# Kernel optimization log

Measured on AMD Instinct MI355X. Metric: run time of the kernel, lower is better.

## Reference

```python
import jax, jax.numpy as jnp
import numpy as np

NI = 2048   # num_items
H = 1024    # hidden_size per direction
B = 256     # batch
T = 256     # max seq len


def setup_inputs() -> dict:
    key = jax.random.key(0)
    ks = jax.random.split(key, 12)
    # ragged lengths, contiguous end-padding with 0 (pack_padded_sequence semantics)
    lens = jax.random.randint(ks[0], (B,), 1, T + 1)
    items = jax.random.randint(ks[1], (B, T), 1, NI)      # 0 is padding, valid in [1, NI)
    actions = jax.random.randint(ks[2], (B, T), 1, 3)     # 1=wrong, 2=right
    valid = jnp.arange(T)[None, :] < lens[:, None]
    items = jnp.where(valid, items, 0)
    actions = jnp.where(valid, actions, 0)
    targets = jax.random.randint(ks[3], (B,), 0, 2)
    s = 0.05
    # W_ih stored transposed [2*NI, 4H]: rows [0:NI) for item one-hot, [NI:2NI) for action one-hot
    Wt_f = jax.random.normal(ks[4], (2 * NI, 4 * H), jnp.float32) * s
    Whh_f = jax.random.normal(ks[5], (H, 4 * H), jnp.float32) * s   # stored as h @ Whh
    b_f = jax.random.normal(ks[6], (4 * H,), jnp.float32) * s       # b_ih + b_hh combined
    Wt_b = jax.random.normal(ks[7], (2 * NI, 4 * H), jnp.float32) * s
    Whh_b = jax.random.normal(ks[8], (H, 4 * H), jnp.float32) * s
    b_b = jax.random.normal(ks[9], (4 * H,), jnp.float32) * s
    Wfc = jax.random.normal(ks[10], (2 * H, 2), jnp.float32) * s
    bfc = jax.random.normal(ks[11], (2,), jnp.float32) * s
    return {"items": items, "actions": actions, "targets": targets,
            "Wt_f": Wt_f, "Whh_f": Whh_f, "b_f": b_f,
            "Wt_b": Wt_b, "Whh_b": Whh_b, "b_b": b_b,
            "Wfc": Wfc, "bfc": bfc}


def _lstm_dir(items, actions, lens, Wt, Whh, b, reverse):
    # one_hot(items) @ W_ih.T == gather rows of W_ih.T  (no dense one-hot materialized)
    Bn, Tn = items.shape
    Hn = Whh.shape[0]
    valid = jnp.arange(Tn)[:, None] < lens[None, :]   # [T, B]
    it, ac = items.T, actions.T                        # [T, B]
    if reverse:
        it, ac, valid = it[::-1], ac[::-1], valid[::-1]

    def step(carry, xs):
        h, c = carry
        i_t, a_t, v = xs
        x = Wt[i_t] + Wt[NI + a_t] + b                 # [B, 4H]
        g = x + h @ Whh
        i, f, gg, o = jnp.split(g, 4, axis=-1)         # PyTorch gate order i,f,g,o
        i, f, o = jax.nn.sigmoid(i), jax.nn.sigmoid(f), jax.nn.sigmoid(o)
        c_new = f * c + i * jnp.tanh(gg)
        h_new = o * jnp.tanh(c_new)
        vm = v[:, None]
        # packed semantics: padded steps are not processed -> state frozen
        return (jnp.where(vm, h_new, h), jnp.where(vm, c_new, c)), None

    h0 = jnp.zeros((Bn, Hn), Wt.dtype)
    (h, _), _ = jax.lax.scan(step, (h0, h0), (it, ac, valid))
    return h  # final hidden: last valid step (fwd) / step 0 (bwd)


def reference(items, actions, targets, Wt_f, Whh_f, b_f, Wt_b, Whh_b, b_b, Wfc, bfc):
    lens = (items != 0).sum(1)
    hf = _lstm_dir(items, actions, lens, Wt_f, Whh_f, b_f, False)
    hb = _lstm_dir(items, actions, lens, Wt_b, Whh_b, b_b, True)
    h = jnp.stack([hf, hb])                            # [2, B, H] like torch h
    # F.dropout(p=0.5, training=True), deterministic key for reproducibility
    keep = jax.random.bernoulli(jax.random.key(42), 0.5, h.shape)
    h = jnp.where(keep, h * 2.0, 0.0)
    feat = jnp.concatenate([h[0], h[1]], axis=-1)      # [B, 2H]
    logits = feat @ Wfc + bfc                          # [B, 2]
    logp = jax.nn.log_softmax(logits, axis=-1)
    loss = -jnp.take_along_axis(logp, targets[:, None], axis=1).mean()
    return loss
```

## Files before the change

kernel.cpp:

```cpp
#include <hip/hip_runtime.h>
#include <stdint.h>

typedef uint32_t u32;
typedef __bf16 bf16;
typedef bf16 bf16x8 __attribute__((ext_vector_type(8)));
typedef float f32x4 __attribute__((ext_vector_type(4)));

#define B_ 256
#define T_ 256
#define H_ 1024
#define G_ 4096
#define NI_ 2048

static constexpr size_t OFF_W2T = 0;
static constexpr size_t SZ_W2T  = (size_t)2 * G_ * H_ * 2;
static constexpr size_t OFF_H   = OFF_W2T + SZ_W2T;
static constexpr size_t SZ_H    = (size_t)2 * 2 * B_ * H_ * 2;
static constexpr size_t OFF_LENS= OFF_H + SZ_H;
static constexpr size_t OFF_RL  = OFF_LENS + 1024;
static constexpr size_t OFF_BAR = OFF_RL + 1024;
static constexpr size_t SZ_BAR  = 36864 * 4;

static constexpr int LDS_BYTES = 131072;

__device__ __forceinline__ float bf2f(uint16_t b){ return __uint_as_float(((u32)b) << 16); }
__device__ __forceinline__ uint16_t f2bf(float f){
  u32 u = __float_as_uint(f);
  return (uint16_t)((u + 0x7fffu + ((u >> 16) & 1u)) >> 16);
}
__device__ __forceinline__ float sigm(float x){ return 1.f / (1.f + __expf(-x)); }
__device__ __forceinline__ float tanh_(float x){ return 1.f - 2.f / (__expf(2.f * x) + 1.f); }

__device__ __forceinline__ void threefry(u32 k0, u32 k1, u32 x0, u32 x1, u32& o0, u32& o1){
  u32 ks2 = k0 ^ k1 ^ 0x1BD11BDAu;
  x0 += k0; x1 += k1;
#define TFR(r) { x0 += x1; x1 = (x1 << r) | (x1 >> (32 - r)); x1 ^= x0; }
  TFR(13) TFR(15) TFR(26) TFR(6)  x0 += k1;  x1 += ks2 + 1u;
  TFR(17) TFR(29) TFR(16) TFR(24) x0 += ks2; x1 += k0 + 2u;
  TFR(13) TFR(15) TFR(26) TFR(6)  x0 += k0;  x1 += k1 + 3u;
  TFR(17) TFR(29) TFR(16) TFR(24) x0 += k1;  x1 += ks2 + 4u;
  TFR(13) TFR(15) TFR(26) TFR(6)  x0 += ks2; x1 += k0 + 5u;
#undef TFR
  o0 = x0; o1 = x1;
}

__device__ __forceinline__ bool keep_mask(u32 idx){
  u32 o0, o1; threefry(0u, 42u, 0u, idx, o0, o1);
  return ((o0 ^ o1) & 0x80000000u) == 0u;
}

__global__ __launch_bounds__(256) void k_prep_w(const float* __restrict__ whh_f,
                                                const float* __restrict__ whh_b,
                                                uint16_t* __restrict__ w2t){
  int bid = blockIdx.x;
  int d  = bid >> 12;
  int r  = bid & 4095;
  int kt = r >> 7;
  int ct = r & 127;
  const float* W = d ? whh_b : whh_f;
  __shared__ float tile[32][33];
  int tid = threadIdx.x;
  int lr = tid >> 5, lc = tid & 31;
#pragma unroll
  for (int i = 0; i < 4; i++)
    tile[lr + i*8][lc] = W[(size_t)(kt*32 + lr + i*8) * G_ + ct*32 + lc];
  __syncthreads();
  int colLocal = tid >> 3, kseg = tid & 7;
  int col = ct*32 + colLocal;
  int strip = col >> 10;
  int hcol  = col & 1023;
  int vcg = (hcol >> 4)*64 + strip*16 + (hcol & 15);
  size_t base = ((size_t)d * G_ + vcg) * H_ + kt*32 + kseg*4;
  u32 w0 = (u32)f2bf(tile[kseg*4+0][colLocal]) | ((u32)f2bf(tile[kseg*4+1][colLocal]) << 16);
  u32 w1 = (u32)f2bf(tile[kseg*4+2][colLocal]) | ((u32)f2bf(tile[kseg*4+3][colLocal]) << 16);
  uint2 v; v.x = w0; v.y = w1;
  *(uint2*)(w2t + base) = v;
}

__global__ __launch_bounds__(256) void k_init(uint16_t* __restrict__ hbuf,
                                              int* __restrict__ lens,
                                              u32* __restrict__ bar,
                                              const int* __restrict__ items){
  int bid = blockIdx.x, tid = threadIdx.x;
  if (bid == 256){
    int cnt = 0;
    for (int t = 0; t < T_; t++) cnt += (items[(size_t)tid * T_ + t] != 0) ? 1 : 0;
    lens[tid] = cnt;
    return;
  }
  size_t g = (size_t)bid * 256 + tid;
  ((uint4*)hbuf)[g] = make_uint4(0,0,0,0);
  if (tid < 36)
    ((uint4*)bar)[bid*36 + tid] = make_uint4(0,0,0,0);
}

#define A_LOAD(dst, base, IMM) \
  asm volatile("global_load_dwordx4 %0, %1, off offset:%2 sc0 sc1" \
    : "=v"(dst) : "v"(base), "i"(IMM) : "memory")
#define A_WAIT(N, r0, r1) \
  asm volatile("s_waitcnt vmcnt(%2)" : "+v"(r0), "+v"(r1) : "i"(N) : "memory")
#define AISS(j) { A_LOAD(pre0[(j)&15], p0, (j)*64); A_LOAD(pre1[(j)&15], p1, (j)*64); }

#define KS1(kk,st,bb) { \
  acc0[st] = __builtin_amdgcn_mfma_f32_16x16x32_bf16(a0_, bb, acc0[st], 0,0,0); \
  acc1[st] = __builtin_amdgcn_mfma_f32_16x16x32_bf16(a1_, bb, acc1[st], 0,0,0); }

#define KSTEP(kk) { \
  bf16x8 bb0 = *(const bf16x8*)(smem + qoff00 + (((kk)&1)?qd1:qd0) + (((kk)&30)<<6)); \
  bf16x8 bb1 = *(const bf16x8*)(smem + qoff00 + 32768  + (((kk)&1)?qd1:qd0) + (((kk)&30)<<6)); \
  bf16x8 bb2 = *(const bf16x8*)(smem + qoff00 + 65536  + (((kk)&1)?qd1:qd0) + (((kk)&30)<<6)); \
  bf16x8 bb3 = *(const bf16x8*)(smem + qoff00 + 98304  + (((kk)&1)?qd1:qd0) + (((kk)&30)<<6)); \
  A_WAIT(((kk)<=16 ? 30 : 62-2*(kk)), pre0[(kk)&15], pre1[(kk)&15]); \
  bf16x8 a0_ = pre0[(kk)&15]; bf16x8 a1_ = pre1[(kk)&15]; \
  KS1(kk,0,bb0) KS1(kk,1,bb1) KS1(kk,2,bb2) KS1(kk,3,bb3) \
  if ((kk) < 16) { AISS((kk)+16); } }

#define R4(M,a) M(a) M((a)+1) M((a)+2) M((a)+3)
#define R16(M,a) R4(M,a) R4(M,(a)+4) R4(M,(a)+8) R4(M,(a)+12)

__global__ __launch_bounds__(256, 1) void k_persist(
    const int* __restrict__ items, const int* __restrict__ actions,
    const float* __restrict__ wt_f, const float* __restrict__ wt_b,
    const float* __restrict__ bias_f, const float* __restrict__ bias_b,
    const uint16_t* __restrict__ w2t, uint16_t* __restrict__ hbuf,
    const int* __restrict__ lens, u32* __restrict__ bar)
{
  extern __shared__ char smem[];
  const int bid = blockIdx.x;
  const int d = bid >> 7;
  const int m = (bid >> 6) & 1;
  const int n = bid & 63;
  const int tid = threadIdx.x;
  const int b0 = m * 128;
  const int ncol = n * 16;
  const float* wt   = d ? wt_b : wt_f;
  const float* bias = d ? bias_b : bias_f;

  {
    const char* wsrc = (const char*)(w2t + ((size_t)d * G_ + n*64) * H_);
#pragma unroll
    for (int i = 0; i < 32; i++){
      int u = i*256 + tid;
      int row = u >> 7, seg = u & 127;
      int sb = seg * 16;
      uint4 v = *(const uint4*)(wsrc + row*2048 + sb);
      *(uint4*)(smem + row*2048 + (sb ^ ((row & 7) << 4))) = v;
    }
  }

  const int w  = tid >> 6;
  const int l  = tid & 63;
  const int c  = l & 15;
  const int lk = l >> 4;
  const int gc = ncol + c;

  float xav[3][4];
#pragma unroll
  for (int a = 0; a < 3; a++)
#pragma unroll
    for (int st = 0; st < 4; st++)
      xav[a][st] = wt[(size_t)(NI_ + a) * G_ + st*1024 + gc] + bias[st*1024 + gc];

  int len_r[8];
#pragma unroll
  for (int i = 0; i < 8; i++)
    len_r[i] = lens[b0 + w*32 + (i>>2)*16 + lk*4 + (i&3)];

  int it_c[8], ac_c[8];
  const int t0 = d ? (T_-1) : 0;
#pragma unroll
  for (int i = 0; i < 8; i++){
    int row = b0 + w*32 + (i>>2)*16 + lk*4 + (i&3);
    it_c[i] = items[(size_t)row * T_ + t0];
    ac_c[i] = actions[(size_t)row * T_ + t0];
  }

  const int key  = (c & 7) << 4;
  const int kbit = (c >> 2) & 1;
  const u32 qoff00 = (u32)(c*2048 + ((lk*16) ^ (key & 48)));
  const u32 qd0 = (u32)((kbit) << 6);
  const u32 qd1 = (u32)((1 ^ kbit) << 6);

  float c_reg[8]; uint16_t h_reg[8];
#pragma unroll
  for (int i = 0; i < 8; i++){ c_reg[i] = 0.f; h_reg[i] = 0; }

  __syncthreads();

  bf16x8 pre0[16], pre1[16];

  for (int s = 0; s < T_; s++){
    const int t = d ? (T_-1-s) : s;

    f32x4 acc0[4], acc1[4];
#pragma unroll
    for (int r4 = 0; r4 < 4; r4++){
      const float* w0r = wt + (size_t)it_c[r4]   * G_ + gc;
      const float* w1r = wt + (size_t)it_c[4+r4] * G_ + gc;
#pragma unroll
      for (int st = 0; st < 4; st++){
        acc0[st][r4] = w0r[st*1024] + xav[ac_c[r4]][st];
        acc1[st][r4] = w1r[st*1024] + xav[ac_c[4+r4]][st];
      }
    }
    __builtin_amdgcn_sched_barrier(0);

    const uint16_t* hin  = hbuf + ((size_t)((s&1)*2 + d)) * B_ * H_;
    uint16_t*       hout = hbuf + ((size_t)(((s&1)^1)*2 + d)) * B_ * H_;
    const char* p0 = (const char*)hin + (size_t)(b0 + w*32 + c)*2048 + lk*16;
    const char* p1 = p0 + 16*2048;

    R16(AISS, 0)
    R16(KSTEP, 0)
    R16(KSTEP, 16)
    __builtin_amdgcn_sched_barrier(0);

    int tn = d ? (t > 0 ? t-1 : 0) : (t < T_-1 ? t+1 : t);
#pragma unroll
    for (int mi = 0; mi < 2; mi++)
#pragma unroll
      for (int r4 = 0; r4 < 4; r4++){
        int i8 = mi*4 + r4;
        int row = b0 + w*32 + mi*16 + lk*4 + r4;
        float g0 = mi ? acc1[0][r4] : acc0[0][r4];
        float g1 = mi ? acc1[1][r4] : acc0[1][r4];
        float g2 = mi ? acc1[2][r4] : acc0[2][r4];
        float g3 = mi ? acc1[3][r4] : acc0[3][r4];
        if (t < len_r[i8]){
          float i_ = sigm(g0);
          float f_ = sigm(g1);
          float gg = tanh_(g2);
          float o_ = sigm(g3);
          float cn = f_ * c_reg[i8] + i_ * gg;
          c_reg[i8] = cn;
          h_reg[i8] = f2bf(o_ * tanh_(cn));
        }
        const uint16_t* addr = hout + (size_t)row * H_ + gc;
        u32 hv = h_reg[i8];
        asm volatile("global_store_short %0, %1, off sc0 sc1" :: "v"(addr), "v"(hv) : "memory");
      }
    asm volatile("s_waitcnt vmcnt(0)" ::: "memory");
    __syncthreads();
    if (s == T_-1) break;

    u32* arr = bar + ((u32)s*8 + (u32)(bid & 7))*16;
    u32* fin = bar + 32768 + (u32)s*16;
    if (tid == 0){
      u32 old = __hip_atomic_fetch_add(arr, 1u, __ATOMIC_RELEASE, __HIP_MEMORY_SCOPE_AGENT);
      if (old == 31u)
        __hip_atomic_fetch_add(fin, 1u, __ATOMIC_RELEASE, __HIP_MEMORY_SCOPE_AGENT);
    }
#pragma unroll
    for (int i = 0; i < 8; i++){
      int row = b0 + w*32 + (i>>2)*16 + lk*4 + (i&3);
      it_c[i] = items[(size_t)row * T_ + tn];
      ac_c[i] = actions[(size_t)row * T_ + tn];
    }
    if (tid == 0){
      while (__hip_atomic_load(fin, __ATOMIC_RELAXED, __HIP_MEMORY_SCOPE_AGENT) < 8u)
        __builtin_amdgcn_s_sleep(2);
    }
    __syncthreads();
  }
}

__global__ __launch_bounds__(256) void k_fc(const uint16_t* __restrict__ hfin,
    const float* __restrict__ wfc, const float* __restrict__ bfc,
    const int* __restrict__ targets, float* __restrict__ rowloss){
  int b = blockIdx.x, tid = threadIdx.x;
  float a0 = 0.f, a1 = 0.f;
  for (int jj = tid; jj < 2*H_; jj += 256){
    int d = jj >> 10, j = jj & 1023;
    float h = bf2f(hfin[(size_t)d * B_ * H_ + (size_t)b * H_ + j]);
    u32 idx = (u32)(d * (B_ * H_) + b * H_ + j);
    float feat = keep_mask(idx) ? (2.f * h) : 0.f;
    a0 += feat * wfc[jj*2 + 0];
    a1 += feat * wfc[jj*2 + 1];
  }
#pragma unroll
  for (int off = 32; off > 0; off >>= 1){
    a0 += __shfl_down(a0, off, 64);
    a1 += __shfl_down(a1, off, 64);
  }
  __shared__ float r0[4], r1[4];
  if ((tid & 63) == 0){ r0[tid >> 6] = a0; r1[tid >> 6] = a1; }
  __syncthreads();
  if (tid == 0){
    float l0 = r0[0]+r0[1]+r0[2]+r0[3] + bfc[0];
    float l1 = r1[0]+r1[1]+r1[2]+r1[3] + bfc[1];
    float mx = fmaxf(l0, l1);
    float lse = mx + logf(__expf(l0 - mx) + __expf(l1 - mx));
    rowloss[b] = lse - (targets[b] ? l1 : l0);
  }
}

__global__ __launch_bounds__(256) void k_loss(const float* __restrict__ rowloss, float* __restrict__ out){
  int tid = threadIdx.x;
  float v = rowloss[tid];
#pragma unroll
  for (int off = 32; off > 0; off >>= 1) v += __shfl_down(v, off, 64);
  __shared__ float r[4];
  if ((tid & 63) == 0) r[tid >> 6] = v;
  __syncthreads();
  if (tid == 0) out[0] = (r[0] + r[1] + r[2] + r[3]) * (1.f / B_);
}

extern "C" void kernel_launch(void* const* d_in, const int* in_sizes, int n_in,
                              void* d_out, int out_size, void* d_ws, size_t ws_size,
                              hipStream_t stream){
  (void)in_sizes; (void)n_in; (void)out_size; (void)ws_size;
  const int*   items   = (const int*)  d_in[0];
  const int*   actions = (const int*)  d_in[1];
  const int*   targets = (const int*)  d_in[2];
  const float* wt_f    = (const float*)d_in[3];
  const float* whh_f   = (const float*)d_in[4];
  const float* b_f     = (const float*)d_in[5];
  const float* wt_b    = (const float*)d_in[6];
  const float* whh_b   = (const float*)d_in[7];
  const float* b_b     = (const float*)d_in[8];
  const float* wfc     = (const float*)d_in[9];
  const float* bfc     = (const float*)d_in[10];

  char* ws = (char*)d_ws;
  uint16_t* w2t   = (uint16_t*)(ws + OFF_W2T);
  uint16_t* hbuf  = (uint16_t*)(ws + OFF_H);
  int*      lens  = (int*)     (ws + OFF_LENS);
  float*    rlbuf = (float*)   (ws + OFF_RL);
  u32*      bar   = (u32*)     (ws + OFF_BAR);

  hipFuncSetAttribute((const void*)k_persist,
                      hipFuncAttributeMaxDynamicSharedMemorySize, LDS_BYTES);

  hipLaunchKernelGGL(k_prep_w, dim3(8192), dim3(256), 0, stream, whh_f, whh_b, w2t);
  hipLaunchKernelGGL(k_init,   dim3(257),  dim3(256), 0, stream, hbuf, lens, bar, items);

  void* args[] = { (void*)&items, (void*)&actions, (void*)&wt_f, (void*)&wt_b,
                   (void*)&b_f, (void*)&b_b, (void*)&w2t, (void*)&hbuf,
                   (void*)&lens, (void*)&bar };
  hipLaunchCooperativeKernel((const void*)k_persist, dim3(256), dim3(256),
                             args, LDS_BYTES, stream);

  hipLaunchKernelGGL(k_fc,   dim3(256), dim3(256), 0, stream, hbuf, wfc, bfc, targets, rlbuf);
  hipLaunchKernelGGL(k_loss, dim3(1),   dim3(256), 0, stream, rlbuf, (float*)d_out);
}
```

Measured before the change: 4.443 ms.

## Use per-step hidden buffers with non-coherent loads and prefetch input gathers ahead

When the workspace is large enough, each timestep writes its hidden state to a fresh buffer, so each step reads an address that has not been written earlier in the launch. That lets the recurrent h loads drop the sc0/sc1 cache-bypass bits and use normal cached loads. The W_ih row gather for the next step is now issued one step early, and item/action indices two steps early, so they overlap the barrier wait instead of the next step's start. The h prefetch depth also drops from 16 to 12 registers. The cost is about 270 MB of extra workspace and a reliance on cross-XCD cache behaviour for correctness, with the old ping-pong path kept as a fallback.

```diff
diff --git a/kernel.cpp b/kernel.cpp
--- a/kernel.cpp
+++ b/kernel.cpp
@@ -14,12 +14,14 @@
 
 static constexpr size_t OFF_W2T = 0;
 static constexpr size_t SZ_W2T  = (size_t)2 * G_ * H_ * 2;
-static constexpr size_t OFF_H   = OFF_W2T + SZ_W2T;
-static constexpr size_t SZ_H    = (size_t)2 * 2 * B_ * H_ * 2;
-static constexpr size_t OFF_LENS= OFF_H + SZ_H;
+static constexpr size_t OFF_LENS= OFF_W2T + SZ_W2T;
 static constexpr size_t OFF_RL  = OFF_LENS + 1024;
 static constexpr size_t OFF_BAR = OFF_RL + 1024;
 static constexpr size_t SZ_BAR  = 36864 * 4;
+static constexpr size_t OFF_H   = OFF_BAR + SZ_BAR;
+static constexpr size_t SZ_H_PP   = (size_t)2 * 2 * B_ * H_ * 2;
+static constexpr size_t SZ_H_DEEP = (size_t)257 * 2 * B_ * H_ * 2;
+static constexpr size_t NEED_DEEP = OFF_H + SZ_H_DEEP;
 
 static constexpr int LDS_BYTES = 131072;
 
@@ -94,30 +96,38 @@
     ((uint4*)bar)[bid*36 + tid] = make_uint4(0,0,0,0);
 }
 
-#define A_LOAD(dst, base, IMM) \
+#define A_LOADC(dst, base, IMM) \
   asm volatile("global_load_dwordx4 %0, %1, off offset:%2 sc0 sc1" \
+    : "=v"(dst) : "v"(base), "i"(IMM) : "memory")
+#define A_LOADN(dst, base, IMM) \
+  asm volatile("global_load_dwordx4 %0, %1, off offset:%2" \
     : "=v"(dst) : "v"(base), "i"(IMM) : "memory")
 #define A_WAIT(N, r0, r1) \
   asm volatile("s_waitcnt vmcnt(%2)" : "+v"(r0), "+v"(r1) : "i"(N) : "memory")
-#define AISS(j) { A_LOAD(pre0[(j)&15], p0, (j)*64); A_LOAD(pre1[(j)&15], p1, (j)*64); }
+#define AISS(j) { if constexpr (DEEP) { \
+    A_LOADN(pre0[(j)%12], p0, (j)*64); A_LOADN(pre1[(j)%12], p1, (j)*64); \
+  } else { \
+    A_LOADC(pre0[(j)%12], p0, (j)*64); A_LOADC(pre1[(j)%12], p1, (j)*64); } }
 
 #define KS1(kk,st,bb) { \
   acc0[st] = __builtin_amdgcn_mfma_f32_16x16x32_bf16(a0_, bb, acc0[st], 0,0,0); \
   acc1[st] = __builtin_amdgcn_mfma_f32_16x16x32_bf16(a1_, bb, acc1[st], 0,0,0); }
 
 #define KSTEP(kk) { \
-  bf16x8 bb0 = *(const bf16x8*)(smem + qoff00 + (((kk)&1)?qd1:qd0) + (((kk)&30)<<6)); \
+  bf16x8 bb0 = *(const bf16x8*)(smem + qoff00 +          (((kk)&1)?qd1:qd0) + (((kk)&30)<<6)); \
   bf16x8 bb1 = *(const bf16x8*)(smem + qoff00 + 32768  + (((kk)&1)?qd1:qd0) + (((kk)&30)<<6)); \
   bf16x8 bb2 = *(const bf16x8*)(smem + qoff00 + 65536  + (((kk)&1)?qd1:qd0) + (((kk)&30)<<6)); \
   bf16x8 bb3 = *(const bf16x8*)(smem + qoff00 + 98304  + (((kk)&1)?qd1:qd0) + (((kk)&30)<<6)); \
-  A_WAIT(((kk)<=16 ? 30 : 62-2*(kk)), pre0[(kk)&15], pre1[(kk)&15]); \
-  bf16x8 a0_ = pre0[(kk)&15]; bf16x8 a1_ = pre1[(kk)&15]; \
+  A_WAIT(((kk)<=20 ? 22 : 62-2*(kk)), pre0[(kk)%12], pre1[(kk)%12]); \
+  bf16x8 a0_ = pre0[(kk)%12]; bf16x8 a1_ = pre1[(kk)%12]; \
   KS1(kk,0,bb0) KS1(kk,1,bb1) KS1(kk,2,bb2) KS1(kk,3,bb3) \
-  if ((kk) < 16) { AISS((kk)+16); } }
+  if ((kk) < 20) { AISS((kk)+12); } }
 
 #define R4(M,a) M(a) M((a)+1) M((a)+2) M((a)+3)
+#define R12(M,a) R4(M,a) R4(M,(a)+4) R4(M,(a)+8)
 #define R16(M,a) R4(M,a) R4(M,(a)+4) R4(M,(a)+8) R4(M,(a)+12)
 
+template <bool DEEP>
 __global__ __launch_bounds__(256, 1) void k_persist(
     const int* __restrict__ items, const int* __restrict__ actions,
     const float* __restrict__ wt_f, const float* __restrict__ wt_b,
@@ -154,25 +164,43 @@
   const int lk = l >> 4;
   const int gc = ncol + c;
 
-  float xav[3][4];
-#pragma unroll
-  for (int a = 0; a < 3; a++)
-#pragma unroll
-    for (int st = 0; st < 4; st++)
-      xav[a][st] = wt[(size_t)(NI_ + a) * G_ + st*1024 + gc] + bias[st*1024 + gc];
+  float xav0[4], xav1[4], xav2[4];
+#pragma unroll
+  for (int st = 0; st < 4; st++){
+    xav0[st] = wt[(size_t)(NI_ + 0) * G_ + st*1024 + gc] + bias[st*1024 + gc];
+    xav1[st] = wt[(size_t)(NI_ + 1) * G_ + st*1024 + gc] + bias[st*1024 + gc];
+    xav2[st] = wt[(size_t)(NI_ + 2) * G_ + st*1024 + gc] + bias[st*1024 + gc];
+  }
 
   int len_r[8];
 #pragma unroll
   for (int i = 0; i < 8; i++)
     len_r[i] = lens[b0 + w*32 + (i>>2)*16 + lk*4 + (i&3)];
 
-  int it_c[8], ac_c[8];
-  const int t0 = d ? (T_-1) : 0;
-#pragma unroll
-  for (int i = 0; i < 8; i++){
-    int row = b0 + w*32 + (i>>2)*16 + lk*4 + (i&3);
-    it_c[i] = items[(size_t)row * T_ + t0];
-    ac_c[i] = actions[(size_t)row * T_ + t0];
+  int itB[8], acB[8], acA[8];
+  float xg[8][4];
+  {
+    const int ta = d ? (T_-1) : 0;
+#pragma unroll
+    for (int i = 0; i < 8; i++){
+      int row = b0 + w*32 + (i>>2)*16 + lk*4 + (i&3);
+      itB[i] = items[(size_t)row * T_ + ta];
+      acB[i] = actions[(size_t)row * T_ + ta];
+    }
+#pragma unroll
+    for (int i = 0; i < 8; i++){
+      const float* wr = wt + (size_t)itB[i] * G_ + gc;
+#pragma unroll
+      for (int st = 0; st < 4; st++) xg[i][st] = wr[st*1024];
+      acA[i] = acB[i];
+    }
+    const int tb = d ? (T_-2) : 1;
+#pragma unroll
+    for (int i = 0; i < 8; i++){
+      int row = b0 + w*32 + (i>>2)*16 + lk*4 + (i&3);
+      itB[i] = items[(size_t)row * T_ + tb];
+      acB[i] = actions[(size_t)row * T_ + tb];
+    }
   }
 
   const int key  = (c & 7) << 4;
@@ -187,7 +215,7 @@
 
   __syncthreads();
 
-  bf16x8 pre0[16], pre1[16];
+  bf16x8 pre0[12], pre1[12];
 
   for (int s = 0; s < T_; s++){
     const int t = d ? (T_-1-s) : s;
@@ -195,27 +223,29 @@
     f32x4 acc0[4], acc1[4];
 #pragma unroll
     for (int r4 = 0; r4 < 4; r4++){
-      const float* w0r = wt + (size_t)it_c[r4]   * G_ + gc;
-      const float* w1r = wt + (size_t)it_c[4+r4] * G_ + gc;
 #pragma unroll
       for (int st = 0; st < 4; st++){
-        acc0[st][r4] = w0r[st*1024] + xav[ac_c[r4]][st];
-        acc1[st][r4] = w1r[st*1024] + xav[ac_c[4+r4]][st];
+        float xa0 = (acA[r4]   == 0) ? xav0[st] : ((acA[r4]   == 1) ? xav1[st] : xav2[st]);
+        float xa1 = (acA[4+r4] == 0) ? xav0[st] : ((acA[4+r4] == 1) ? xav1[st] : xav2[st]);
+        acc0[st][r4] = xg[r4][st]   + xa0;
+        acc1[st][r4] = xg[4+r4][st] + xa1;
       }
     }
+    asm volatile("s_waitcnt vmcnt(0)" ::: "memory");
     __builtin_amdgcn_sched_barrier(0);
 
-    const uint16_t* hin  = hbuf + ((size_t)((s&1)*2 + d)) * B_ * H_;
-    uint16_t*       hout = hbuf + ((size_t)(((s&1)^1)*2 + d)) * B_ * H_;
+    const size_t bin  = DEEP ? (size_t)(s*2 + d)       : (size_t)((s&1)*2 + d);
+    const size_t bout = DEEP ? (size_t)((s+1)*2 + d)   : (size_t)(((s&1)^1)*2 + d);
+    const uint16_t* hin  = hbuf + bin  * (size_t)(B_*H_);
+    uint16_t*       hout = hbuf + bout * (size_t)(B_*H_);
     const char* p0 = (const char*)hin + (size_t)(b0 + w*32 + c)*2048 + lk*16;
     const char* p1 = p0 + 16*2048;
 
-    R16(AISS, 0)
+    R12(AISS, 0)
     R16(KSTEP, 0)
     R16(KSTEP, 16)
     __builtin_amdgcn_sched_barrier(0);
 
-    int tn = d ? (t > 0 ? t-1 : 0) : (t < T_-1 ? t+1 : t);
 #pragma unroll
     for (int mi = 0; mi < 2; mi++)
 #pragma unroll
@@ -252,9 +282,21 @@
     }
 #pragma unroll
     for (int i = 0; i < 8; i++){
-      int row = b0 + w*32 + (i>>2)*16 + lk*4 + (i&3);
-      it_c[i] = items[(size_t)row * T_ + tn];
-      ac_c[i] = actions[(size_t)row * T_ + tn];
+      const float* wr = wt + (size_t)itB[i] * G_ + gc;
+#pragma unroll
+      for (int st = 0; st < 4; st++) xg[i][st] = wr[st*1024];
+      acA[i] = acB[i];
+    }
+    {
+      int t2 = d ? (T_-1-(s+2)) : (s+2);
+      if (t2 < 0) t2 = 0;
+      if (t2 > T_-1) t2 = T_-1;
+#pragma unroll
+      for (int i = 0; i < 8; i++){
+        int row = b0 + w*32 + (i>>2)*16 + lk*4 + (i&3);
+        itB[i] = items[(size_t)row * T_ + t2];
+        acB[i] = actions[(size_t)row * T_ + t2];
+      }
     }
     if (tid == 0){
       while (__hip_atomic_load(fin, __ATOMIC_RELAXED, __HIP_MEMORY_SCOPE_AGENT) < 8u)
@@ -308,7 +350,7 @@
 extern "C" void kernel_launch(void* const* d_in, const int* in_sizes, int n_in,
                               void* d_out, int out_size, void* d_ws, size_t ws_size,
                               hipStream_t stream){
-  (void)in_sizes; (void)n_in; (void)out_size; (void)ws_size;
+  (void)in_sizes; (void)n_in; (void)out_size;
   const int*   items   = (const int*)  d_in[0];
   const int*   actions = (const int*)  d_in[1];
   const int*   targets = (const int*)  d_in[2];
@@ -323,12 +365,16 @@
 
   char* ws = (char*)d_ws;
   uint16_t* w2t   = (uint16_t*)(ws + OFF_W2T);
-  uint16_t* hbuf  = (uint16_t*)(ws + OFF_H);
   int*      lens  = (int*)     (ws + OFF_LENS);
   float*    rlbuf = (float*)   (ws + OFF_RL);
   u32*      bar   = (u32*)     (ws + OFF_BAR);
-
-  hipFuncSetAttribute((const void*)k_persist,
+  uint16_t* hbuf  = (uint16_t*)(ws + OFF_H);
+
+  const bool deep = (ws_size >= NEED_DEEP);
+
+  hipFuncSetAttribute((const void*)k_persist<true>,
+                      hipFuncAttributeMaxDynamicSharedMemorySize, LDS_BYTES);
+  hipFuncSetAttribute((const void*)k_persist<false>,
                       hipFuncAttributeMaxDynamicSharedMemorySize, LDS_BYTES);
 
   hipLaunchKernelGGL(k_prep_w, dim3(8192), dim3(256), 0, stream, whh_f, whh_b, w2t);
@@ -337,9 +383,14 @@
   void* args[] = { (void*)&items, (void*)&actions, (void*)&wt_f, (void*)&wt_b,
                    (void*)&b_f, (void*)&b_b, (void*)&w2t, (void*)&hbuf,
                    (void*)&lens, (void*)&bar };
-  hipLaunchCooperativeKernel((const void*)k_persist, dim3(256), dim3(256),
-                             args, LDS_BYTES, stream);
-
-  hipLaunchKernelGGL(k_fc,   dim3(256), dim3(256), 0, stream, hbuf, wfc, bfc, targets, rlbuf);
+  if (deep)
+    hipLaunchCooperativeKernel((const void*)k_persist<true>, dim3(256), dim3(256),
+                               args, LDS_BYTES, stream);
+  else
+    hipLaunchCooperativeKernel((const void*)k_persist<false>, dim3(256), dim3(256),
+                               args, LDS_BYTES, stream);
+
+  const uint16_t* hfin = hbuf + (deep ? (size_t)512 * B_ * H_ : 0);
+  hipLaunchKernelGGL(k_fc,   dim3(256), dim3(256), 0, stream, hfin, wfc, bfc, targets, rlbuf);
   hipLaunchKernelGGL(k_loss, dim3(1),   dim3(256), 0, stream, rlbuf, (float*)d_out);
 }
```

Result: slower. 4.680 ms (+5.3%).

## Interleave both LSTM directions per block with per-group flag sync and ring-buffered h

Applied to the files above, without the earlier changes.

Each persistent block now handles both the forward and backward direction over half as many gate columns, alternating between them each step. This lets one direction's recurrent GEMM overlap the other's barrier wait. The global two-level atomic barrier is replaced by per-block step flags polled only within the same batch-half group. The hidden state moves to a column-blocked layout held in a ring of R slots sized to the workspace, so h loads can drop the sc0/sc1 cache bypass and rely on periodic agent-scope acquire fences. In exchange there is more register pressure, a more complex layout, correctness that depends on the fence period and ring depth, and reliance on ws_size.

```diff
diff --git a/kernel.cpp b/kernel.cpp
--- a/kernel.cpp
+++ b/kernel.cpp
@@ -14,12 +14,13 @@
 
 static constexpr size_t OFF_W2T = 0;
 static constexpr size_t SZ_W2T  = (size_t)2 * G_ * H_ * 2;
-static constexpr size_t OFF_H   = OFF_W2T + SZ_W2T;
-static constexpr size_t SZ_H    = (size_t)2 * 2 * B_ * H_ * 2;
-static constexpr size_t OFF_LENS= OFF_H + SZ_H;
+static constexpr size_t OFF_LENS= OFF_W2T + SZ_W2T;
 static constexpr size_t OFF_RL  = OFF_LENS + 1024;
 static constexpr size_t OFF_BAR = OFF_RL + 1024;
-static constexpr size_t SZ_BAR  = 36864 * 4;
+static constexpr size_t SZ_BAR  = 4096;
+static constexpr size_t OFF_H   = OFF_BAR + SZ_BAR;
+static constexpr size_t SZ_SLOT = (size_t)B_ * H_ * 2;
+static constexpr size_t SLOT_U16 = (size_t)B_ * H_;
 
 static constexpr int LDS_BYTES = 131072;
 
@@ -69,7 +70,7 @@
   int col = ct*32 + colLocal;
   int strip = col >> 10;
   int hcol  = col & 1023;
-  int vcg = (hcol >> 4)*64 + strip*16 + (hcol & 15);
+  int vcg = (hcol >> 3)*32 + (strip & 1)*16 + (strip >> 1)*8 + (hcol & 7);
   size_t base = ((size_t)d * G_ + vcg) * H_ + kt*32 + kseg*4;
   u32 w0 = (u32)f2bf(tile[kseg*4+0][colLocal]) | ((u32)f2bf(tile[kseg*4+1][colLocal]) << 16);
   u32 w1 = (u32)f2bf(tile[kseg*4+2][colLocal]) | ((u32)f2bf(tile[kseg*4+3][colLocal]) << 16);
@@ -77,7 +78,8 @@
   *(uint2*)(w2t + base) = v;
 }
 
-__global__ __launch_bounds__(256) void k_init(uint16_t* __restrict__ hbuf,
+__global__ __launch_bounds__(256) void k_init(uint16_t* __restrict__ hfp,
+                                              uint16_t* __restrict__ hbp,
                                               int* __restrict__ lens,
                                               u32* __restrict__ bar,
                                               const int* __restrict__ items){
@@ -88,91 +90,159 @@
     lens[tid] = cnt;
     return;
   }
-  size_t g = (size_t)bid * 256 + tid;
-  ((uint4*)hbuf)[g] = make_uint4(0,0,0,0);
-  if (tid < 36)
-    ((uint4*)bar)[bid*36 + tid] = make_uint4(0,0,0,0);
-}
-
-#define A_LOAD(dst, base, IMM) \
+  size_t g = (size_t)(bid & 127) * 256 + tid;
+  uint16_t* hp = (bid < 128) ? hfp : hbp;
+  ((uint4*)hp)[g] = make_uint4(0,0,0,0);
+  if (bid == 0) ((uint4*)bar)[tid] = make_uint4(0,0,0,0);
+}
+
+#define A_LOADC(dst, base, IMM) \
   asm volatile("global_load_dwordx4 %0, %1, off offset:%2 sc0 sc1" \
+    : "=v"(dst) : "v"(base), "i"(IMM) : "memory")
+#define A_LOADN(dst, base, IMM) \
+  asm volatile("global_load_dwordx4 %0, %1, off offset:%2" \
     : "=v"(dst) : "v"(base), "i"(IMM) : "memory")
 #define A_WAIT(N, r0, r1) \
   asm volatile("s_waitcnt vmcnt(%2)" : "+v"(r0), "+v"(r1) : "i"(N) : "memory")
-#define AISS(j) { A_LOAD(pre0[(j)&15], p0, (j)*64); A_LOAD(pre1[(j)&15], p1, (j)*64); }
-
-#define KS1(kk,st,bb) { \
-  acc0[st] = __builtin_amdgcn_mfma_f32_16x16x32_bf16(a0_, bb, acc0[st], 0,0,0); \
-  acc1[st] = __builtin_amdgcn_mfma_f32_16x16x32_bf16(a1_, bb, acc1[st], 0,0,0); }
+#define AISS(j) { if constexpr (CACHED) { \
+    A_LOADN(pre0[(j)%10], pA + (size_t)(j)*16384, 0); \
+    A_LOADN(pre1[(j)%10], pA + (size_t)(j)*16384, 256); \
+  } else { \
+    A_LOADC(pre0[(j)%10], pA + (size_t)(j)*16384, 0); \
+    A_LOADC(pre1[(j)%10], pA + (size_t)(j)*16384, 256); } }
 
 #define KSTEP(kk) { \
-  bf16x8 bb0 = *(const bf16x8*)(smem + qoff00 + (((kk)&1)?qd1:qd0) + (((kk)&30)<<6)); \
-  bf16x8 bb1 = *(const bf16x8*)(smem + qoff00 + 32768  + (((kk)&1)?qd1:qd0) + (((kk)&30)<<6)); \
-  bf16x8 bb2 = *(const bf16x8*)(smem + qoff00 + 65536  + (((kk)&1)?qd1:qd0) + (((kk)&30)<<6)); \
-  bf16x8 bb3 = *(const bf16x8*)(smem + qoff00 + 98304  + (((kk)&1)?qd1:qd0) + (((kk)&30)<<6)); \
-  A_WAIT(((kk)<=16 ? 30 : 62-2*(kk)), pre0[(kk)&15], pre1[(kk)&15]); \
-  bf16x8 a0_ = pre0[(kk)&15]; bf16x8 a1_ = pre1[(kk)&15]; \
-  KS1(kk,0,bb0) KS1(kk,1,bb1) KS1(kk,2,bb2) KS1(kk,3,bb3) \
-  if ((kk) < 16) { AISS((kk)+16); } }
-
-#define R4(M,a) M(a) M((a)+1) M((a)+2) M((a)+3)
+  bf16x8 bb0 = *(const bf16x8*)(smemD +         qoff00 + (((kk)&1)?qd1:qd0) + (((kk)&30)<<6)); \
+  bf16x8 bb1 = *(const bf16x8*)(smemD + 32768 + qoff00 + (((kk)&1)?qd1:qd0) + (((kk)&30)<<6)); \
+  A_WAIT(((kk)<=21 ? 18 : 62-2*(kk)), pre0[(kk)%10], pre1[(kk)%10]); \
+  bf16x8 a0_ = pre0[(kk)%10]; bf16x8 a1_ = pre1[(kk)%10]; \
+  accT0[0] = __builtin_amdgcn_mfma_f32_16x16x32_bf16(a0_, bb0, accT0[0], 0,0,0); \
+  accT0[1] = __builtin_amdgcn_mfma_f32_16x16x32_bf16(a1_, bb0, accT0[1], 0,0,0); \
+  accT1[0] = __builtin_amdgcn_mfma_f32_16x16x32_bf16(a0_, bb1, accT1[0], 0,0,0); \
+  accT1[1] = __builtin_amdgcn_mfma_f32_16x16x32_bf16(a1_, bb1, accT1[1], 0,0,0); \
+  if ((kk) < 22) { AISS((kk)+10); } }
+
+#define R2(M,a)  M(a) M((a)+1)
+#define R4(M,a)  M(a) M((a)+1) M((a)+2) M((a)+3)
+#define R10(M,a) R4(M,a) R4(M,(a)+4) R2(M,(a)+8)
 #define R16(M,a) R4(M,a) R4(M,(a)+4) R4(M,(a)+8) R4(M,(a)+12)
 
+#define DO_DIR(SMOFF, HINP, HOUTP, XG, XAV, ACV, TT, CREG, HREG, FOFF) \
+  { \
+    f32x4 accT0[2], accT1[2]; \
+    _Pragma("unroll") for (int mi = 0; mi < 2; mi++) \
+    _Pragma("unroll") for (int r4 = 0; r4 < 4; r4++){ \
+      int i8 = mi*4 + r4; int a_ = ACV[i8]; \
+      accT0[mi][r4] = XG[i8][0] + XAV[a_][0]; \
+      accT1[mi][r4] = XG[i8][1] + XAV[a_][1]; } \
+    asm volatile("s_waitcnt vmcnt(0)" ::: "memory"); \
+    __builtin_amdgcn_sched_barrier(0); \
+    const char* pA = (const char*)(HINP) + (size_t)(b0 + w*32 + c)*16 + (size_t)lk*4096; \
+    const char* smemD = smem + (SMOFF); \
+    R10(AISS, 0) \
+    R16(KSTEP, 0) R16(KSTEP, 16) \
+    __builtin_amdgcn_sched_barrier(0); \
+    _Pragma("unroll") for (int mi = 0; mi < 2; mi++) \
+    _Pragma("unroll") for (int r4 = 0; r4 < 4; r4++){ \
+      int i8 = mi*4 + r4; \
+      float u0 = accT0[mi][r4], u1 = accT1[mi][r4]; \
+      float v0 = __shfl_xor(u0, 8, 64), v1 = __shfl_xor(u1, 8, 64); \
+      float gi = chi ? v0 : u0; \
+      float gf = chi ? v1 : u1; \
+      float gg = chi ? u0 : v0; \
+      float go = chi ? u1 : v1; \
+      int row = b0 + w*32 + mi*16 + lk*4 + r4; \
+      if ((TT) < len_r[i8]){ \
+        float i_ = sigm(gi), f_ = sigm(gf), g_ = tanh_(gg), o_ = sigm(go); \
+        float cn = f_ * CREG[i8] + i_ * g_; \
+        CREG[i8] = cn; HREG[i8] = f2bf(o_ * tanh_(cn)); } \
+      if (!chi){ \
+        const uint16_t* addr_ = (HOUTP) + (size_t)n*2048 + (size_t)row*8 + hc8; \
+        u32 hv_ = HREG[i8]; \
+        asm volatile("global_store_short %0, %1, off sc0 sc1" :: "v"(addr_), "v"(hv_) : "memory"); } \
+    } \
+    asm volatile("s_waitcnt vmcnt(0)" ::: "memory"); \
+  } \
+  __syncthreads(); \
+  if (tid == 0) __hip_atomic_store(bar + (FOFF) + n, (u32)(s+1), __ATOMIC_RELAXED, __HIP_MEMORY_SCOPE_AGENT);
+
+#define WAITGRP(FOFF, TGT) do { \
+  if (tid < 64){ \
+    const u32 tgt_ = (u32)(TGT); \
+    u32* fp_ = bar + (FOFF); \
+    for(;;){ \
+      u32 va_ = __hip_atomic_load(fp_ + tid,      __ATOMIC_RELAXED, __HIP_MEMORY_SCOPE_AGENT); \
+      u32 vb_ = __hip_atomic_load(fp_ + tid + 64, __ATOMIC_RELAXED, __HIP_MEMORY_SCOPE_AGENT); \
+      if (__all(va_ >= tgt_ && vb_ >= tgt_)) break; \
+      __builtin_amdgcn_s_sleep(1); \
+    } \
+  } \
+  __syncthreads(); \
+} while(0)
+
+template <bool CACHED>
 __global__ __launch_bounds__(256, 1) void k_persist(
     const int* __restrict__ items, const int* __restrict__ actions,
     const float* __restrict__ wt_f, const float* __restrict__ wt_b,
     const float* __restrict__ bias_f, const float* __restrict__ bias_b,
-    const uint16_t* __restrict__ w2t, uint16_t* __restrict__ hbuf,
-    const int* __restrict__ lens, u32* __restrict__ bar)
+    const uint16_t* __restrict__ w2t, uint16_t* __restrict__ hf, uint16_t* __restrict__ hb,
+    const int* __restrict__ lens, u32* __restrict__ bar, int rmask)
 {
   extern __shared__ char smem[];
   const int bid = blockIdx.x;
-  const int d = bid >> 7;
-  const int m = (bid >> 6) & 1;
-  const int n = bid & 63;
+  const int m = (bid >> 2) & 1;
+  const int n = (bid >> 3) * 4 + (bid & 3);
   const int tid = threadIdx.x;
   const int b0 = m * 128;
-  const int ncol = n * 16;
-  const float* wt   = d ? wt_b : wt_f;
-  const float* bias = d ? bias_b : bias_f;
-
-  {
-    const char* wsrc = (const char*)(w2t + ((size_t)d * G_ + n*64) * H_);
-#pragma unroll
-    for (int i = 0; i < 32; i++){
+
+#pragma unroll
+  for (int dd = 0; dd < 2; dd++){
+    const char* wsrc = (const char*)(w2t + ((size_t)dd * G_ + n*32) * H_);
+#pragma unroll
+    for (int i = 0; i < 16; i++){
       int u = i*256 + tid;
       int row = u >> 7, seg = u & 127;
       int sb = seg * 16;
       uint4 v = *(const uint4*)(wsrc + row*2048 + sb);
-      *(uint4*)(smem + row*2048 + (sb ^ ((row & 7) << 4))) = v;
+      *(uint4*)(smem + dd*65536 + row*2048 + (sb ^ ((row & 7) << 4))) = v;
     }
   }
 
-  const int w  = tid >> 6;
-  const int l  = tid & 63;
-  const int c  = l & 15;
-  const int lk = l >> 4;
-  const int gc = ncol + c;
-
-  float xav[3][4];
-#pragma unroll
-  for (int a = 0; a < 3; a++)
-#pragma unroll
-    for (int st = 0; st < 4; st++)
-      xav[a][st] = wt[(size_t)(NI_ + a) * G_ + st*1024 + gc] + bias[st*1024 + gc];
+  const int w   = tid >> 6;
+  const int l   = tid & 63;
+  const int c   = l & 15;
+  const int lk  = l >> 4;
+  const int hc8 = c & 7;
+  const int chi = (c >> 3) & 1;
+  const int gcol0 = (chi ? 2 : 0)*1024 + n*8 + hc8;
+  const int gcol1 = (chi ? 3 : 1)*1024 + n*8 + hc8;
+
+  float xavf[3][2], xavb[3][2];
+#pragma unroll
+  for (int a = 0; a < 3; a++){
+    xavf[a][0] = wt_f[(size_t)(NI_ + a) * G_ + gcol0] + bias_f[gcol0];
+    xavf[a][1] = wt_f[(size_t)(NI_ + a) * G_ + gcol1] + bias_f[gcol1];
+    xavb[a][0] = wt_b[(size_t)(NI_ + a) * G_ + gcol0] + bias_b[gcol0];
+    xavb[a][1] = wt_b[(size_t)(NI_ + a) * G_ + gcol1] + bias_b[gcol1];
+  }
 
   int len_r[8];
 #pragma unroll
   for (int i = 0; i < 8; i++)
     len_r[i] = lens[b0 + w*32 + (i>>2)*16 + lk*4 + (i&3)];
 
-  int it_c[8], ac_c[8];
-  const int t0 = d ? (T_-1) : 0;
+  int itf[8], acf[8], itb[8], acb[8];
+  float xgf[8][2], xgb[8][2];
 #pragma unroll
   for (int i = 0; i < 8; i++){
     int row = b0 + w*32 + (i>>2)*16 + lk*4 + (i&3);
-    it_c[i] = items[(size_t)row * T_ + t0];
-    ac_c[i] = actions[(size_t)row * T_ + t0];
+    itf[i] = items[(size_t)row * T_ + 0];        acf[i] = actions[(size_t)row * T_ + 0];
+    itb[i] = items[(size_t)row * T_ + (T_-1)];   acb[i] = actions[(size_t)row * T_ + (T_-1)];
+  }
+#pragma unroll
+  for (int i = 0; i < 8; i++){
+    xgf[i][0] = wt_f[(size_t)itf[i] * G_ + gcol0]; xgf[i][1] = wt_f[(size_t)itf[i] * G_ + gcol1];
+    xgb[i][0] = wt_b[(size_t)itb[i] * G_ + gcol0]; xgb[i][1] = wt_b[(size_t)itb[i] * G_ + gcol1];
   }
 
   const int key  = (c & 7) << 4;
@@ -181,97 +251,57 @@
   const u32 qd0 = (u32)((kbit) << 6);
   const u32 qd1 = (u32)((1 ^ kbit) << 6);
 
-  float c_reg[8]; uint16_t h_reg[8];
-#pragma unroll
-  for (int i = 0; i < 8; i++){ c_reg[i] = 0.f; h_reg[i] = 0; }
+  float crf[8], crb[8]; uint16_t hrf[8], hrb[8];
+#pragma unroll
+  for (int i = 0; i < 8; i++){ crf[i] = 0.f; crb[i] = 0.f; hrf[i] = 0; hrb[i] = 0; }
 
   __syncthreads();
 
-  bf16x8 pre0[16], pre1[16];
+  bf16x8 pre0[10], pre1[10];
 
   for (int s = 0; s < T_; s++){
-    const int t = d ? (T_-1-s) : s;
-
-    f32x4 acc0[4], acc1[4];
-#pragma unroll
-    for (int r4 = 0; r4 < 4; r4++){
-      const float* w0r = wt + (size_t)it_c[r4]   * G_ + gc;
-      const float* w1r = wt + (size_t)it_c[4+r4] * G_ + gc;
-#pragma unroll
-      for (int st = 0; st < 4; st++){
-        acc0[st][r4] = w0r[st*1024] + xav[ac_c[r4]][st];
-        acc1[st][r4] = w1r[st*1024] + xav[ac_c[4+r4]][st];
+    if (CACHED && s != 0 && ((s & rmask) == 0))
+      __builtin_amdgcn_fence(__ATOMIC_ACQUIRE, "agent");
+
+    const int tf = s, tb = T_-1-s;
+    const uint16_t* hfin  = hf + (size_t)(s & rmask) * SLOT_U16;
+    uint16_t*       hfout = hf + (size_t)((s+1) & rmask) * SLOT_U16;
+    const uint16_t* hbin  = hb + (size_t)(s & rmask) * SLOT_U16;
+    uint16_t*       hbout = hb + (size_t)((s+1) & rmask) * SLOT_U16;
+
+    DO_DIR(0, hfin, hfout, xgf, xavf, acf, tf, crf, hrf, m*128)
+    if (s) { WAITGRP(256 + m*128, (u32)s); }
+    DO_DIR(65536, hbin, hbout, xgb, xavb, acb, tb, crb, hrb, 256 + m*128)
+    if (s == T_-1) break;
+
+    {
+      int tf2 = s + 1, tb2 = T_ - 2 - s;
+#pragma unroll
+      for (int i = 0; i < 8; i++){
+        int row = b0 + w*32 + (i>>2)*16 + lk*4 + (i&3);
+        itf[i] = items[(size_t)row * T_ + tf2]; acf[i] = actions[(size_t)row * T_ + tf2];
+        itb[i] = items[(size_t)row * T_ + tb2]; acb[i] = actions[(size_t)row * T_ + tb2];
+      }
+#pragma unroll
+      for (int i = 0; i < 8; i++){
+        xgf[i][0] = wt_f[(size_t)itf[i] * G_ + gcol0]; xgf[i][1] = wt_f[(size_t)itf[i] * G_ + gcol1];
+        xgb[i][0] = wt_b[(size_t)itb[i] * G_ + gcol0]; xgb[i][1] = wt_b[(size_t)itb[i] * G_ + gcol1];
       }
     }
-    __builtin_amdgcn_sched_barrier(0);
-
-    const uint16_t* hin  = hbuf + ((size_t)((s&1)*2 + d)) * B_ * H_;
-    uint16_t*       hout = hbuf + ((size_t)(((s&1)^1)*2 + d)) * B_ * H_;
-    const char* p0 = (const char*)hin + (size_t)(b0 + w*32 + c)*2048 + lk*16;
-    const char* p1 = p0 + 16*2048;
-
-    R16(AISS, 0)
-    R16(KSTEP, 0)
-    R16(KSTEP, 16)
-    __builtin_amdgcn_sched_barrier(0);
-
-    int tn = d ? (t > 0 ? t-1 : 0) : (t < T_-1 ? t+1 : t);
-#pragma unroll
-    for (int mi = 0; mi < 2; mi++)
-#pragma unroll
-      for (int r4 = 0; r4 < 4; r4++){
-        int i8 = mi*4 + r4;
-        int row = b0 + w*32 + mi*16 + lk*4 + r4;
-        float g0 = mi ? acc1[0][r4] : acc0[0][r4];
-        float g1 = mi ? acc1[1][r4] : acc0[1][r4];
-        float g2 = mi ? acc1[2][r4] : acc0[2][r4];
-        float g3 = mi ? acc1[3][r4] : acc0[3][r4];
-        if (t < len_r[i8]){
-          float i_ = sigm(g0);
-          float f_ = sigm(g1);
-          float gg = tanh_(g2);
-          float o_ = sigm(g3);
-          float cn = f_ * c_reg[i8] + i_ * gg;
-          c_reg[i8] = cn;
-          h_reg[i8] = f2bf(o_ * tanh_(cn));
-        }
-        const uint16_t* addr = hout + (size_t)row * H_ + gc;
-        u32 hv = h_reg[i8];
-        asm volatile("global_store_short %0, %1, off sc0 sc1" :: "v"(addr), "v"(hv) : "memory");
-      }
-    asm volatile("s_waitcnt vmcnt(0)" ::: "memory");
-    __syncthreads();
-    if (s == T_-1) break;
-
-    u32* arr = bar + ((u32)s*8 + (u32)(bid & 7))*16;
-    u32* fin = bar + 32768 + (u32)s*16;
-    if (tid == 0){
-      u32 old = __hip_atomic_fetch_add(arr, 1u, __ATOMIC_RELEASE, __HIP_MEMORY_SCOPE_AGENT);
-      if (old == 31u)
-        __hip_atomic_fetch_add(fin, 1u, __ATOMIC_RELEASE, __HIP_MEMORY_SCOPE_AGENT);
-    }
-#pragma unroll
-    for (int i = 0; i < 8; i++){
-      int row = b0 + w*32 + (i>>2)*16 + lk*4 + (i&3);
-      it_c[i] = items[(size_t)row * T_ + tn];
-      ac_c[i] = actions[(size_t)row * T_ + tn];
-    }
-    if (tid == 0){
-      while (__hip_atomic_load(fin, __ATOMIC_RELAXED, __HIP_MEMORY_SCOPE_AGENT) < 8u)
-        __builtin_amdgcn_s_sleep(2);
-    }
-    __syncthreads();
-  }
-}
-
-__global__ __launch_bounds__(256) void k_fc(const uint16_t* __restrict__ hfin,
+    WAITGRP(m*128, (u32)(s+1));
+  }
+}
+
+__global__ __launch_bounds__(256) void k_fc(const uint16_t* __restrict__ hfq,
+    const uint16_t* __restrict__ hbq,
     const float* __restrict__ wfc, const float* __restrict__ bfc,
     const int* __restrict__ targets, float* __restrict__ rowloss){
   int b = blockIdx.x, tid = threadIdx.x;
   float a0 = 0.f, a1 = 0.f;
   for (int jj = tid; jj < 2*H_; jj += 256){
     int d = jj >> 10, j = jj & 1023;
-    float h = bf2f(hfin[(size_t)d * B_ * H_ + (size_t)b * H_ + j]);
+    const uint16_t* hp = d ? hbq : hfq;
+    float h = bf2f(hp[(size_t)(j >> 3) * 2048 + (size_t)b * 8 + (j & 7)]);
     u32 idx = (u32)(d * (B_ * H_) + b * H_ + j);
     float feat = keep_mask(idx) ? (2.f * h) : 0.f;
     a0 += feat * wfc[jj*2 + 0];
@@ -308,7 +338,7 @@
 extern "C" void kernel_launch(void* const* d_in, const int* in_sizes, int n_in,
                               void* d_out, int out_size, void* d_ws, size_t ws_size,
                               hipStream_t stream){
-  (void)in_sizes; (void)n_in; (void)out_size; (void)ws_size;
+  (void)in_sizes; (void)n_in; (void)out_size;
   const int*   items   = (const int*)  d_in[0];
   const int*   actions = (const int*)  d_in[1];
   const int*   targets = (const int*)  d_in[2];
@@ -323,23 +353,37 @@
 
   char* ws = (char*)d_ws;
   uint16_t* w2t   = (uint16_t*)(ws + OFF_W2T);
-  uint16_t* hbuf  = (uint16_t*)(ws + OFF_H);
   int*      lens  = (int*)     (ws + OFF_LENS);
   float*    rlbuf = (float*)   (ws + OFF_RL);
   u32*      bar   = (u32*)     (ws + OFF_BAR);
-
-  hipFuncSetAttribute((const void*)k_persist,
+  uint16_t* hf    = (uint16_t*)(ws + OFF_H);
+
+  int R = 0;
+  if      (ws_size >= OFF_H + 32u * SZ_SLOT) R = 16;
+  else if (ws_size >= OFF_H + 16u * SZ_SLOT) R = 8;
+  else if (ws_size >= OFF_H +  8u * SZ_SLOT) R = 4;
+  int rmask = R ? (R - 1) : 1;
+  int Reff  = R ? R : 2;
+  uint16_t* hb = hf + (size_t)Reff * SLOT_U16;
+
+  hipFuncSetAttribute((const void*)k_persist<true>,
                       hipFuncAttributeMaxDynamicSharedMemorySize, LDS_BYTES);
+  hipFuncSetAttribute((const void*)k_persist<false>,
+                      hipFuncAttributeMaxDynamicSharedMemorySize, LDS_BYTES);
 
   hipLaunchKernelGGL(k_prep_w, dim3(8192), dim3(256), 0, stream, whh_f, whh_b, w2t);
-  hipLaunchKernelGGL(k_init,   dim3(257),  dim3(256), 0, stream, hbuf, lens, bar, items);
+  hipLaunchKernelGGL(k_init,   dim3(257),  dim3(256), 0, stream, hf, hb, lens, bar, items);
 
   void* args[] = { (void*)&items, (void*)&actions, (void*)&wt_f, (void*)&wt_b,
-                   (void*)&b_f, (void*)&b_b, (void*)&w2t, (void*)&hbuf,
-                   (void*)&lens, (void*)&bar };
-  hipLaunchCooperativeKernel((const void*)k_persist, dim3(256), dim3(256),
-                             args, LDS_BYTES, stream);
-
-  hipLaunchKernelGGL(k_fc,   dim3(256), dim3(256), 0, stream, hbuf, wfc, bfc, targets, rlbuf);
+                   (void*)&b_f, (void*)&b_b, (void*)&w2t, (void*)&hf, (void*)&hb,
+                   (void*)&lens, (void*)&bar, (void*)&rmask };
+  if (R)
+    hipLaunchCooperativeKernel((const void*)k_persist<true>, dim3(256), dim3(256),
+                               args, LDS_BYTES, stream);
+  else
+    hipLaunchCooperativeKernel((const void*)k_persist<false>, dim3(256), dim3(256),
+                               args, LDS_BYTES, stream);
+
+  hipLaunchKernelGGL(k_fc,   dim3(256), dim3(256), 0, stream, hf, hb, wfc, bfc, targets, rlbuf);
   hipLaunchKernelGGL(k_loss, dim3(1),   dim3(256), 0, stream, rlbuf, (float*)d_out);
 }
```

Result: faster. 3.642 ms (-18.0%).
